# Performance work log

Hardware: AMD Instinct MI355X
Metric: run time of the kernel (lower is better)

The kernel has to match this reference:

```python
import jax, jax.numpy as jnp
import numpy as np

A_DIM = 18
HID = 512
LSTM_IN = HID + A_DIM + 1  # 531


def setup_inputs() -> dict:
    key = jax.random.key(0)
    ks = jax.random.split(key, 26)
    T, B = 80, 64
    inp = {}
    inp["o"] = jax.random.randint(ks[0], (T, B, 1, 84, 84), 0, 255, dtype=jnp.int32)
    inp["a"] = jax.random.randint(ks[1], (T, B), 0, A_DIM, dtype=jnp.int32)
    inp["r"] = jax.random.normal(ks[2], (T, B), dtype=jnp.float32)
    inp["done"] = jax.random.randint(ks[3], (T, B), 0, 2, dtype=jnp.int32)
    inp["h0"] = jnp.zeros((B, HID), dtype=jnp.float32)
    inp["c0"] = jnp.zeros((B, HID), dtype=jnp.float32)

    def gw(k, shape, s=0.05):
        return (jax.random.normal(k, shape, dtype=jnp.float32) * s)

    # CNN trunk params (torch Conv2d OIHW layout)
    inp["conv1_w"] = gw(ks[4], (32, 1, 8, 8))
    inp["conv1_b"] = jnp.zeros((32,), jnp.float32)
    inp["conv2_w"] = gw(ks[5], (64, 32, 4, 4))
    inp["conv2_b"] = jnp.zeros((64,), jnp.float32)
    inp["conv3_w"] = gw(ks[6], (64, 64, 3, 3))
    inp["conv3_b"] = jnp.zeros((64,), jnp.float32)
    inp["fc_w"] = gw(ks[7], (HID, 64 * 7 * 7))
    inp["fc_b"] = jnp.zeros((HID,), jnp.float32)
    # LSTM params (torch gate order: i, f, g, o)
    inp["W_ih"] = gw(ks[8], (4 * HID, LSTM_IN))
    inp["W_hh"] = gw(ks[9], (4 * HID, HID))
    inp["b_ih"] = jnp.zeros((4 * HID,), jnp.float32)
    inp["b_hh"] = jnp.zeros((4 * HID,), jnp.float32)
    # Dueling heads
    inp["adv_w1"] = gw(ks[10], (HID, HID))
    inp["adv_b1"] = jnp.zeros((HID,), jnp.float32)
    inp["adv_w2"] = gw(ks[11], (A_DIM, HID))
    inp["adv_b2"] = jnp.zeros((A_DIM,), jnp.float32)
    inp["val_w1"] = gw(ks[12], (HID, HID))
    inp["val_b1"] = jnp.zeros((HID,), jnp.float32)
    inp["val_w2"] = gw(ks[13], (1, HID))
    inp["val_b2"] = jnp.zeros((1,), jnp.float32)
    return inp


def _conv(x, w, b, stride):
    y = jax.lax.conv_general_dilated(
        x, w, (stride, stride), 'VALID',
        dimension_numbers=('NCHW', 'OIHW', 'NCHW'))
    return y + b[None, :, None, None]


def reference(o, a, r, done, h0, c0,
              conv1_w, conv1_b, conv2_w, conv2_b, conv3_w, conv3_b,
              fc_w, fc_b, W_ih, W_hh, b_ih, b_hh,
              adv_w1, adv_b1, adv_w2, adv_b2,
              val_w1, val_b1, val_w2, val_b2):
    T, B = o.shape[0], o.shape[1]
    x = o.reshape(T * B, 1, 84, 84).astype(jnp.float32) / 255.0
    x = jax.nn.relu(_conv(x, conv1_w, conv1_b, 4))   # [TB,32,20,20]
    x = jax.nn.relu(_conv(x, conv2_w, conv2_b, 2))   # [TB,64,9,9]
    x = jax.nn.relu(_conv(x, conv3_w, conv3_b, 1))   # [TB,64,7,7]
    x = x.reshape(T * B, 64 * 7 * 7)
    hidden = jax.nn.relu(x @ fc_w.T + fc_b).reshape(T, B, HID)

    a_one_hot = jax.nn.one_hot(a, A_DIM, dtype=jnp.float32)      # [T,B,A]
    lstm_in = jnp.concatenate([hidden, r[..., None], a_one_hot], axis=-1)  # [T,B,531]
    keep = (1.0 - done.astype(jnp.float32))[..., None]           # [T,B,1]
    bias = b_ih + b_hh

    def step(carry, inp_t):
        h, c = carry
        x_t, m = inp_t
        h = h * m
        c = c * m
        g = x_t @ W_ih.T + h @ W_hh.T + bias   # [B, 4H]
        i, f, gg, oo = jnp.split(g, 4, axis=-1)
        c = jax.nn.sigmoid(f) * c + jax.nn.sigmoid(i) * jnp.tanh(gg)
        h = jax.nn.sigmoid(oo) * jnp.tanh(c)
        return (h, c), h

    (hT, cT), hs = jax.lax.scan(step, (h0, c0), (lstm_in, keep))
    z = hs.reshape(T * B, HID)

    adv = jax.nn.relu(z @ adv_w1.T + adv_b1) @ adv_w2.T + adv_b2  # [TB,A]
    val = jax.nn.relu(z @ val_w1.T + val_b1) @ val_w2.T + val_b2  # [TB,1]
    q = val + (adv - adv.mean(axis=1, keepdims=True))
    return q.reshape(T, B, A_DIM), hT, cT
```

## Files before the change

### kernel.cpp

```cpp
#include <hip/hip_runtime.h>
#include <hip/hip_bf16.h>
#include <stdint.h>

typedef __bf16 bf16;
typedef __bf16 bfrag __attribute__((ext_vector_type(8)));
typedef short s16x8 __attribute__((ext_vector_type(8)));
typedef float f32x4 __attribute__((ext_vector_type(4)));
typedef float f32x16 __attribute__((ext_vector_type(16)));
typedef uint32_t u32x4 __attribute__((ext_vector_type(4)));

#define DEV __device__ __forceinline__

DEV bfrag ldg16(const bf16* p){ return *(const bfrag*)p; }

struct U64x2 { uint64_t a, b; };
DEV bfrag ld2x8(const bf16* p){
  U64x2 t; t.a = *(const uint64_t*)p; t.b = *(const uint64_t*)(p+4);
  return __builtin_bit_cast(bfrag, t);
}

DEV f32x4  mfma16(bfrag a, bfrag b, f32x4  c){ return __builtin_amdgcn_mfma_f32_16x16x32_bf16(a,b,c,0,0,0); }
DEV f32x16 mfma32(bfrag a, bfrag b, f32x16 c){ return __builtin_amdgcn_mfma_f32_32x32x16_bf16(a,b,c,0,0,0); }

DEV f32x16 zero16(){
  f32x16 v;
  for(int i=0;i<16;++i) v[i]=0.f;
  return v;
}
DEV f32x4 zero4(){
  f32x4 v;
  for(int i=0;i<4;++i) v[i]=0.f;
  return v;
}

DEV float sigm(float x){ return 1.0f/(1.0f+__expf(-x)); }
DEV float ftanh(float x){ float e = __expf(2.f*x); return 1.f - 2.f/(e+1.f); }

DEV u32x4 ldcg4(const uint32_t* p){
  u32x4 r;
  asm volatile("global_load_dwordx4 %0, %1, off sc0 sc1" : "=v"(r) : "v"(p));
  return r;
}

DEV uint32_t pk2f(float a, float b){
  bf16 x = (bf16)a, y = (bf16)b;
  return (uint32_t)__builtin_bit_cast(uint16_t,x) | ((uint32_t)__builtin_bit_cast(uint16_t,y)<<16);
}

DEV void gl_lds16(const bf16* g, void* l){
  __builtin_amdgcn_global_load_lds(
      (const __attribute__((address_space(1))) uint32_t*)g,
      (__attribute__((address_space(3))) uint32_t*)l, 16, 0, 0);
}

__global__ __launch_bounds__(256) void k_prep(
    const float* __restrict__ c1w, const float* __restrict__ c2w,
    const float* __restrict__ c3w, const float* __restrict__ fcw,
    const float* __restrict__ Wih, const float* __restrict__ WhhF,
    const float* __restrict__ bih, const float* __restrict__ bhh,
    const float* __restrict__ aw1, const float* __restrict__ aw2,
    const float* __restrict__ vw1, const float* __restrict__ vw2,
    const float* __restrict__ h0, const float* __restrict__ ab1,
    const float* __restrict__ vb1,
    bf16* w1b, bf16* w2r, bf16* w3r, bf16* fcwr, bf16* Wx, bf16* Whh,
    float* biasL, float* Wr, float* Wa, bf16* headw1, float* headb1,
    bf16* w2cat, uint32_t* hcurT)
{
  long i = (long)blockIdx.x*256 + threadIdx.x;
  if (i < 2048){ int co=(int)(i>>6), k=(int)(i&63);
    w1b[i] = (bf16)(c1w[co*64+k]*(1.f/255.f)); return; } i -= 2048;
  if (i < 32768){ int o=(int)(i>>9), k=(int)(i&511);
    int ky=k>>7, kx=(k>>5)&3, ci=k&31;
    w2r[i] = (bf16)c2w[((o*32+ci)*4+ky)*4+kx]; return; } i -= 32768;
  if (i < 36864){ int o=(int)(i/576), k=(int)(i%576);
    int ky=k/192, rem=k-ky*192, kx=rem>>6, ci=rem&63;
    w3r[i] = (bf16)c3w[((o*64+ci)*3+ky)*3+kx]; return; } i -= 36864;
  if (i < 1605632){
    int o=(int)(i/3136), rem=(int)(i%3136);
    int ci=rem/49, yx=rem-ci*49, y=yx/7, x=yx-y*7;
    fcwr[o*3200 + y*448 + x*64 + ci] = (bf16)fcw[i]; return; } i -= 1605632;
  if (i < 32768){ int o=(int)(i>>6), k=(int)(i&63);
    fcwr[o*3200 + 3136 + k] = (bf16)0.f; return; } i -= 32768;
  if (i < 1048576){ int n=(int)(i>>9), k=(int)(i&511);
    Wx[i] = (bf16)Wih[n*531+k]; return; } i -= 1048576;
  if (i < 1048576){ int n=(int)(i>>9), k=(int)(i&511);
    Whh[i] = (bf16)WhhF[n*512+k]; return; } i -= 1048576;
  if (i < 2048){ biasL[i] = bih[i]+bhh[i]; return; } i -= 2048;
  if (i < 2048){ Wr[i] = Wih[i*531+512]; return; } i -= 2048;
  if (i < 36864){ int j=(int)(i>>11), n=(int)(i&2047);
    Wa[i] = Wih[n*531+513+j]; return; } i -= 36864;
  if (i < 524288){ headw1[i] = (bf16)(i<262144 ? aw1[i] : vw1[i-262144]); return; } i -= 524288;
  if (i < 1024){ headb1[i] = (i<512) ? ab1[i] : vb1[i-512]; return; } i -= 1024;
  if (i < 32768){ int n=(int)(i>>10), k=(int)(i&1023);
    float v = 0.f;
    if (n<18 && k<512) v = aw2[n*512+k];
    else if (n==18 && k>=512) v = vw2[k-512];
    w2cat[i] = (bf16)v; return; } i -= 32768;
  if (i < 32768){
    if (i < 16384){
      int row = (int)(i>>8), wd = (int)(i&255);
      uint32_t pk = pk2f(h0[row*512 + wd*2], h0[row*512 + wd*2 + 1]);
      hcurT[i] = pk & ~0x00010001u;
    } else {
      hcurT[i] = 0x00010000u;
    }
    return;
  }
}

__global__ __launch_bounds__(256,2) void k_conv12(
    const int* __restrict__ o, const bf16* __restrict__ w1b,
    const float* __restrict__ c1b, const bf16* __restrict__ w2r,
    const float* __restrict__ c2b, bf16* __restrict__ act2)
{
  __shared__ bf16 lact[2][16000];
  const int tid = threadIdx.x;
  const int w = tid>>6, l = tid&63;
  const int img = w>>1, h = w&1;
  const long gimg = (long)blockIdx.x*2 + img;
  const int* ip = o + gimg*7056;
  char* lw = (char*)&lact[img][0];
  {
    bfrag bw[4];
    #pragma unroll
    for (int ks=0;ks<4;++ks) bw[ks] = ldg16(w1b + (l&31)*64 + ks*16 + 8*(l>>5));
    const float bias = c1b[l&31];
    for (int mt=h; mt<13; mt+=2){
      f32x16 acc = zero16();
      int m0 = mt*32 + (l&31);
      int p  = m0>399 ? 399 : m0;
      int oy = p/20, ox = p - oy*20;
      #pragma unroll
      for (int ks=0;ks<4;++ks){
        int ky = 2*ks + (l>>5);
        const int* q = ip + (oy*4+ky)*84 + ox*4;
        int4 i0 = *(const int4*)q;
        int4 i1 = *(const int4*)(q+4);
        bfrag a;
        a[0]=(bf16)(float)i0.x; a[1]=(bf16)(float)i0.y;
        a[2]=(bf16)(float)i0.z; a[3]=(bf16)(float)i0.w;
        a[4]=(bf16)(float)i1.x; a[5]=(bf16)(float)i1.y;
        a[6]=(bf16)(float)i1.z; a[7]=(bf16)(float)i1.w;
        acc = mfma32(a, bw[ks], acc);
      }
      #pragma unroll
      for (int r2=0;r2<16;++r2){
        int row = (r2&3) + 8*(r2>>2) + 4*(l>>5);
        int m = mt*32 + row;
        if (m < 400){
          float v = acc[r2] + bias; v = v>0.f ? v : 0.f;
          *(bf16*)(lw + m*80 + (l&31)*2) = (bf16)v;
        }
      }
    }
  }
  __syncthreads();
  {
    f32x16 acc2[3];
    #pragma unroll
    for (int a2=0;a2<3;++a2) acc2[a2]=zero16();
    int pb[3];
    #pragma unroll
    for (int mt=0;mt<3;++mt){
      int m = mt*32 + (l&31); int p = m>80 ? 80 : m;
      int oy = p/9, ox = p - oy*9;
      pb[mt] = (oy*2)*20 + ox*2;
    }
    #pragma unroll 4
    for (int ks=0; ks<32; ++ks){
      int k  = ks*16 + 8*(l>>5);
      int ky = k>>7, kx = (k>>5)&3, ci = k&31;
      bfrag b0 = ldg16(w2r + (32*h + (l&31))*512 + k);
      #pragma unroll
      for (int mt=0; mt<3; ++mt){
        int p2 = pb[mt] + ky*20 + kx;
        bfrag a = *(const bfrag*)(lw + p2*80 + ci*2);
        acc2[mt] = mfma32(a, b0, acc2[mt]);
      }
    }
    const float bias2 = c2b[32*h + (l&31)];
    #pragma unroll
    for (int mt=0; mt<3; ++mt){
      #pragma unroll
      for (int r2=0;r2<16;++r2){
        int row = (r2&3) + 8*(r2>>2) + 4*(l>>5);
        int m = mt*32 + row;
        if (m < 81){
          float v = acc2[mt][r2] + bias2; v = v>0.f ? v : 0.f;
          act2[gimg*5184 + m*64 + 32*h + (l&31)] = (bf16)v;
        }
      }
    }
  }
}

__global__ __launch_bounds__(256,2) void k_conv3(
    const bf16* __restrict__ act2, const bf16* __restrict__ w3r,
    const float* __restrict__ c3b, bf16* __restrict__ act3)
{
  const int tid=threadIdx.x, w=tid>>6, l=tid&63;
  const long img = (long)blockIdx.x*4 + w;
  const bf16* A = act2 + img*5184;
  f32x16 acc[2][2];
  #pragma unroll
  for(int a2=0;a2<2;++a2){ acc[a2][0]=zero16(); acc[a2][1]=zero16(); }
  #pragma unroll 4
  for (int ks=0; ks<36; ++ks){
    int k  = ks*16 + 8*(l>>5);
    int ky = k/192, rem = k - ky*192, kx = rem>>6, ci = rem&63;
    bfrag b0 = ldg16(w3r + (l&31)*576 + k);
    bfrag b1 = ldg16(w3r + (32+(l&31))*576 + k);
    #pragma unroll
    for (int mt=0; mt<2; ++mt){
      int m = mt*32 + (l&31); int p = m>48 ? 48 : m;
      int oy = p/7, ox = p - oy*7;
      bfrag a = ldg16(A + ((oy+ky)*9 + (ox+kx))*64 + ci);
      acc[mt][0] = mfma32(a, b0, acc[mt][0]);
      acc[mt][1] = mfma32(a, b1, acc[mt][1]);
    }
  }
  const float bias0 = c3b[l&31], bias1 = c3b[32+(l&31)];
  #pragma unroll
  for (int mt=0; mt<2; ++mt){
    #pragma unroll
    for (int r2=0;r2<16;++r2){
      int row = (r2&3) + 8*(r2>>2) + 4*(l>>5);
      int m = mt*32 + row;
      if (m < 50){
        float v0 = 0.f, v1 = 0.f;
        if (m < 49){
          v0 = acc[mt][0][r2] + bias0; v0 = v0>0.f ? v0 : 0.f;
          v1 = acc[mt][1][r2] + bias1; v1 = v1>0.f ? v1 : 0.f;
        }
        act3[img*3200 + m*64 + (l&31)]      = (bf16)v0;
        act3[img*3200 + m*64 + 32 + (l&31)] = (bf16)v1;
      }
    }
  }
}

template<bool RELU, bool OUTBF16>
__global__ __launch_bounds__(256,4) void k_gemm(
    const bf16* __restrict__ A, long lda,
    const bf16* __restrict__ W, long ldb,
    const float* __restrict__ bias,
    float* __restrict__ outF, bf16* __restrict__ outB, long ldo, int K,
    const float* __restrict__ fixR, const int* __restrict__ fixA,
    const float* __restrict__ fixWr, const float* __restrict__ fixWa)
{
  __shared__ bf16 sA[8192];
  char* sb = (char*)sA;
  const int tid=threadIdx.x, w=tid>>6, l=tid&63;
  const int m0 = blockIdx.x*64, n0 = blockIdx.y*128;
  f32x16 acc[2]; acc[0]=zero16(); acc[1]=zero16();
  const int mt = w&1;
  const int rowa = mt*32 + (l&31);
  for (int kc=0; kc<K; kc+=128){
    __syncthreads();
    #pragma unroll
    for (int j=0;j<4;++j){
      int idx = j*64 + l;
      int row = w*16 + (idx>>4);
      int seg = idx&15;
      const bf16* gp = A + (long)(m0+row)*lda + kc + (((seg*16) ^ ((row&15)<<4))>>1);
      gl_lds16(gp, sb + w*4096 + j*1024);
    }
    asm volatile("s_waitcnt vmcnt(0)" ::: "memory");
    __syncthreads();
    #pragma unroll
    for (int ks=0; ks<8; ++ks){
      bfrag a = *(const bfrag*)(sb + rowa*256 + ((ks*32 + (l>>5)*16) ^ ((rowa&15)<<4)));
      #pragma unroll
      for (int j=0;j<2;++j){
        int nt = (w>>1)*2 + j;
        bfrag b = ldg16(W + (long)(n0 + nt*32 + (l&31))*ldb + kc + ks*16 + 8*(l>>5));
        acc[j] = mfma32(a, b, acc[j]);
      }
    }
  }
  #pragma unroll
  for (int j=0;j<2;++j){
    int nt = (w>>1)*2 + j;
    int gc = n0 + nt*32 + (l&31);
    float bv = bias ? bias[gc] : 0.f;
    float wrv = fixR ? fixWr[gc] : 0.f;
    #pragma unroll
    for (int r2=0;r2<16;++r2){
      int row = (r2&3) + 8*(r2>>2) + 4*(l>>5);
      long gr = m0 + mt*32 + row;
      float v = acc[j][r2] + bv;
      if (fixR) v += fixR[gr]*wrv + fixWa[(long)fixA[gr]*2048 + gc];
      if (RELU) v = v>0.f ? v : 0.f;
      if (OUTBF16) outB[gr*ldo + gc] = (bf16)v;
      else         outF[gr*ldo + gc] = v;
    }
  }
}

__global__ __launch_bounds__(256,1) void k_lstm(
    const bf16* __restrict__ G, const int* __restrict__ done,
    const float* __restrict__ c0, const bf16* __restrict__ Whh,
    uint32_t* __restrict__ hcurT, bf16* __restrict__ hseq,
    float* __restrict__ outH, float* __restrict__ outC)
{
  __shared__ bf16 sh2[8192];
  __shared__ float sg[4][16][33];
  __shared__ float sc[16][33];
  __shared__ char  sdone[80][16];
  const int tid=threadIdx.x, w=tid>>6, l=tid&63;
  const int blk=blockIdx.x;
  const int grp=(blk&7)>>1, jj=((blk&1)<<3)|(blk>>3);
  const int bb = grp*16, uu = jj*32;

  for (int p=tid; p<512; p+=256){ int m=p>>5, u=p&31; sc[m][u] = c0[(bb+m)*512 + uu + u]; }
  for (int p=tid; p<1280; p+=256){ int t=p>>4, m=p&15; sdone[t][m] = (char)done[t*64 + bb + m]; }

  bfrag wb0[16], wb1[16];
  {
    const long row0 = (long)w*512 + uu + (l&15);
    #pragma unroll
    for (int ks=0; ks<16; ++ks){
      int k = ks*32 + 8*(l>>4);
      wb0[ks] = ldg16(Whh + row0*512 + k);
      wb1[ks] = ldg16(Whh + (row0+16)*512 + k);
      asm volatile("" : "+v"(wb0[ks]), "+v"(wb1[ks]));
    }
  }

  char* shb = (char*)sh2;
  const int loff = l*16;
  const int srow  = tid>>4;
  const int sci   = tid&15;

  __syncthreads();

  for (int t=0; t<80; ++t){
    float gv0[4], gv1[4];
    {
      const bf16* Gt = G + ((long)t*64 + bb)*2048 + w*512 + uu;
      #pragma unroll
      for (int r2=0;r2<4;++r2){
        int m2 = (l>>4)*4 + r2;
        gv0[r2] = (float)Gt[(long)m2*2048 + (l&15)];
        gv1[r2] = (float)Gt[(long)m2*2048 + 16 + (l&15)];
      }
    }
    __builtin_amdgcn_sched_barrier(0);
    {
      const uint32_t* hb = hcurT + (size_t)(t&1)*16384 + (size_t)(bb+srow)*256 + sci*16;
      u32x4 hv[4];
      const uint32_t expPat = ((uint32_t)(t&1)) | (((uint32_t)((t>>1)&1))<<16);
      for (;;){
        #pragma unroll
        for (int j2=0;j2<4;++j2) hv[j2] = ldcg4(hb + j2*4);
        asm volatile("s_waitcnt vmcnt(0)" ::: "memory");
        bool ok = true;
        #pragma unroll
        for (int j2=0;j2<4;++j2){
          ok &= ((hv[j2][0]&0x00010001u)==expPat) & ((hv[j2][1]&0x00010001u)==expPat)
              & ((hv[j2][2]&0x00010001u)==expPat) & ((hv[j2][3]&0x00010001u)==expPat);
        }
        if (__all(ok)) break;
        __builtin_amdgcn_s_sleep(1);
      }
      if (sdone[t][srow]){
        #pragma unroll
        for (int j2=0;j2<4;++j2){ u32x4 z = {0,0,0,0}; hv[j2] = z; }
      } else {
        #pragma unroll
        for (int j2=0;j2<4;++j2){
          hv[j2][0] &= ~0x00010001u; hv[j2][1] &= ~0x00010001u;
          hv[j2][2] &= ~0x00010001u; hv[j2][3] &= ~0x00010001u;
        }
      }
      #pragma unroll
      for (int j=0;j<4;++j){
        *(u32x4*)(shb + sci*1024 + ((((srow + 16*j)*16)) ^ ((sci&7)<<4))) = hv[j];
      }
    }
    __syncthreads();
    f32x4 a0e = zero4(), a0o = zero4(), a1e = zero4(), a1o = zero4();
    #pragma unroll
    for (int ks=0; ks<16; ++ks){
      bfrag a = *(const bfrag*)(shb + ks*1024 + (loff ^ ((ks&7)<<4)));
      if (ks & 1){ a0o = mfma16(a, wb0[ks], a0o); a1o = mfma16(a, wb1[ks], a1o); }
      else       { a0e = mfma16(a, wb0[ks], a0e); a1e = mfma16(a, wb1[ks], a1e); }
    }
    #pragma unroll
    for (int r2=0;r2<4;++r2){
      int m = (l>>4)*4 + r2;
      sg[w][m][(l&15)]    = a0e[r2] + a0o[r2] + gv0[r2];
      sg[w][m][16+(l&15)] = a1e[r2] + a1o[r2] + gv1[r2];
    }
    __syncthreads();
    {
      int p0 = tid*2; int m = p0>>5, u = p0&31;
      int dn = sdone[t][m];
      float c_0 = dn ? 0.f : sc[m][u];
      float c_1 = dn ? 0.f : sc[m][u+1];
      float i0=sg[0][m][u],   f0=sg[1][m][u],   g0=sg[2][m][u],   o0=sg[3][m][u];
      float i1=sg[0][m][u+1], f1=sg[1][m][u+1], g1=sg[2][m][u+1], o1=sg[3][m][u+1];
      float cn0 = sigm(f0)*c_0 + sigm(i0)*ftanh(g0);
      float cn1 = sigm(f1)*c_1 + sigm(i1)*ftanh(g1);
      float h_0 = sigm(o0)*ftanh(cn0);
      float h_1 = sigm(o1)*ftanh(cn1);
      sc[m][u] = cn0; sc[m][u+1] = cn1;
      uint32_t pk = pk2f(h_0, h_1);
      int p1 = (t+1)&3;
      uint32_t pat = ((uint32_t)(p1&1)) | (((uint32_t)(p1>>1))<<16);
      uint32_t pkT = (pk & ~0x00010001u) | pat;
      __hip_atomic_store(
          hcurT + (size_t)((t+1)&1)*16384 + (size_t)(bb+m)*256 + ((uu+u)>>1),
          pkT, __ATOMIC_RELAXED, __HIP_MEMORY_SCOPE_AGENT);
      *(uint32_t*)(hseq + ((long)t*64 + bb + m)*512 + uu + u) = pk;
      if (t == 79){
        outH[(bb+m)*512 + uu + u]   = h_0;  outH[(bb+m)*512 + uu + u+1] = h_1;
        outC[(bb+m)*512 + uu + u]   = cn0;  outC[(bb+m)*512 + uu + u+1] = cn1;
      }
    }
  }
}

__global__ __launch_bounds__(256) void k_qhead(
    const bf16* __restrict__ zav, const bf16* __restrict__ w2cat,
    const float* __restrict__ ab2, const float* __restrict__ vb2,
    float* __restrict__ q)
{
  __shared__ float sq[4][16][33];
  const int tid=threadIdx.x, w=tid>>6, l=tid&63;
  const int s0 = blockIdx.x*64 + w*16;
  f32x4 acc0 = zero4(), acc1 = zero4();
  const int row = l&15;
  #pragma unroll 4
  for (int ks=0; ks<32; ++ks){
    int k = ks*32 + 8*(l>>4);
    bfrag a  = ldg16(zav + (long)(s0+row)*1024 + k);
    bfrag b0 = ldg16(w2cat + (l&15)*1024 + k);
    bfrag b1 = ldg16(w2cat + (16+(l&15))*1024 + k);
    acc0 = mfma16(a, b0, acc0);
    acc1 = mfma16(a, b1, acc1);
  }
  #pragma unroll
  for (int r2=0;r2<4;++r2){
    int m = (l>>4)*4 + r2;
    sq[w][m][l&15]      = acc0[r2];
    sq[w][m][16+(l&15)] = acc1[r2];
  }
  __syncthreads();
  if (l < 16){
    int s = s0 + l;
    float av[18]; float sum = 0.f;
    #pragma unroll
    for (int j=0;j<18;++j){ av[j] = sq[w][l][j] + ab2[j]; sum += av[j]; }
    float val = sq[w][l][18] + vb2[0];
    float mean = sum * (1.f/18.f);
    #pragma unroll
    for (int j=0;j<18;++j) q[(long)s*18 + j] = val + av[j] - mean;
  }
}

extern "C" void kernel_launch(void* const* d_in, const int* in_sizes, int n_in,
                              void* d_out, int out_size, void* d_ws, size_t ws_size,
                              hipStream_t stream)
{
  (void)in_sizes; (void)n_in; (void)out_size;
  const int*   o_in = (const int*)  d_in[0];
  const int*   a_in = (const int*)  d_in[1];
  const float* r_in = (const float*)d_in[2];
  const int*   done = (const int*)  d_in[3];
  const float* h0   = (const float*)d_in[4];
  const float* c0   = (const float*)d_in[5];
  const float* c1w  = (const float*)d_in[6],  *c1b=(const float*)d_in[7];
  const float* c2w  = (const float*)d_in[8],  *c2b=(const float*)d_in[9];
  const float* c3w  = (const float*)d_in[10], *c3b=(const float*)d_in[11];
  const float* fcw  = (const float*)d_in[12], *fcb=(const float*)d_in[13];
  const float* Wih  = (const float*)d_in[14], *WhhF=(const float*)d_in[15];
  const float* bih  = (const float*)d_in[16], *bhh=(const float*)d_in[17];
  const float* aw1  = (const float*)d_in[18], *ab1=(const float*)d_in[19];
  const float* aw2  = (const float*)d_in[20], *ab2=(const float*)d_in[21];
  const float* vw1  = (const float*)d_in[22], *vb1=(const float*)d_in[23];
  const float* vw2  = (const float*)d_in[24], *vb2=(const float*)d_in[25];

  char* ws = (char*)d_ws;
  size_t off = 0;
  auto alloc = [&](size_t b){ size_t p = off; off = (off + b + 255) & ~(size_t)255; return p; };
  bf16*  act2   = (bf16*) (ws + alloc(53084160));
  bf16*  act3   = (bf16*) (ws + alloc(32768000));
  bf16*  hidden = (bf16*) (ws + alloc(5242880));
  uint32_t* hcurT = (uint32_t*)(ws + alloc(131072));
  bf16*  w1b    = (bf16*) (ws + alloc(4096));
  bf16*  w2r    = (bf16*) (ws + alloc(65536));
  bf16*  w3r    = (bf16*) (ws + alloc(73728));
  bf16*  fcwr   = (bf16*) (ws + alloc(3276800));
  bf16*  Wx     = (bf16*) (ws + alloc(2097152));
  bf16*  Whh    = (bf16*) (ws + alloc(2097152));
  float* biasL  = (float*)(ws + alloc(8192));
  float* Wr     = (float*)(ws + alloc(8192));
  float* Wa     = (float*)(ws + alloc(147456));
  bf16*  headw1 = (bf16*) (ws + alloc(1048576));
  float* headb1 = (float*)(ws + alloc(4096));
  bf16*  w2cat  = (bf16*) (ws + alloc(65536));
  if (off > ws_size) return;

  bf16*  G    = act2;
  bf16*  hseq = hidden;
  bf16*  zav  = act3;

  float* qout = (float*)d_out;
  float* outH = qout + 92160;
  float* outC = qout + 124928;

  k_prep<<<17340, 256, 0, stream>>>(c1w, c2w, c3w, fcw, Wih, WhhF, bih, bhh,
      aw1, aw2, vw1, vw2, h0, ab1, vb1, w1b, w2r, w3r, fcwr, Wx, Whh,
      biasL, Wr, Wa, headw1, headb1, w2cat, hcurT);

  k_conv12<<<2560, 256, 0, stream>>>(o_in, w1b, c1b, w2r, c2b, act2);
  k_conv3<<<1280, 256, 0, stream>>>(act2, w3r, c3b, act3);
  k_gemm<true,true><<<dim3(80,4), 256, 0, stream>>>(
      act3, 3200, fcwr, 3200, fcb, nullptr, hidden, 512, 3200,
      nullptr, nullptr, nullptr, nullptr);
  k_gemm<false,true><<<dim3(80,16), 256, 0, stream>>>(
      hidden, 512, Wx, 512, biasL, nullptr, G, 2048, 512,
      r_in, a_in, Wr, Wa);

  k_lstm<<<64, 256, 0, stream>>>(G, done, c0, Whh, hcurT, hseq, outH, outC);

  k_gemm<true,true><<<dim3(80,8), 256, 0, stream>>>(
      hseq, 512, headw1, 512, headb1, nullptr, zav, 1024, 512,
      nullptr, nullptr, nullptr, nullptr);
  k_qhead<<<80, 256, 0, stream>>>(zav, w2cat, ab2, vb2, qout);
}
```

Before: 603.6 us.

## Remap LSTM gate columns per wave to compute cell update in registers

Each wave's MFMA output columns are remapped so that a lane pair (xor 8) holds the i/f and g/o gates for the same hidden unit. The cell state now lives in registers and the gate exchange uses shuffles instead of a shared-memory staging buffer, which removes one __syncthreads per timestep. The h shared buffer is double-buffered by timestep parity so the next step's staging does not race with reads from the current step. In exchange, half the lanes sit idle during the packed stores, and the row ordering of the W_hh and G loads changes.

Result: slower. 754.4 us (median of 2 runs) (+25.0%).

```diff
diff --git a/kernel.cpp b/kernel.cpp
--- a/kernel.cpp
+++ b/kernel.cpp
@@ -303,31 +303,37 @@
     uint32_t* __restrict__ hcurT, bf16* __restrict__ hseq,
     float* __restrict__ outH, float* __restrict__ outC)
 {
-  __shared__ bf16 sh2[8192];
-  __shared__ float sg[4][16][33];
-  __shared__ float sc[16][33];
+  __shared__ bf16 sh2[2][8192];
   __shared__ char  sdone[80][16];
   const int tid=threadIdx.x, w=tid>>6, l=tid&63;
   const int blk=blockIdx.x;
   const int grp=(blk&7)>>1, jj=((blk&1)<<3)|(blk>>3);
   const int bb = grp*16, uu = jj*32;
-
-  for (int p=tid; p<512; p+=256){ int m=p>>5, u=p&31; sc[m][u] = c0[(bb+m)*512 + uu + u]; }
+  const int w8 = w*8;
+  const int x  = l&15;
+
   for (int p=tid; p<1280; p+=256){ int t=p>>4, m=p&15; sdone[t][m] = (char)done[t*64 + bb + m]; }
+
+  float creg[4];
+  #pragma unroll
+  for (int r2=0;r2<4;++r2){
+    int m = (l>>4)*4 + r2;
+    creg[r2] = c0[(bb+m)*512 + uu + w8 + (x&7)];
+  }
 
   bfrag wb0[16], wb1[16];
   {
-    const long row0 = (long)w*512 + uu + (l&15);
+    const long row0 = (long)((x>>3))*512 + uu + w8 + (x&7);
+    const long row1 = row0 + 1024;
     #pragma unroll
     for (int ks=0; ks<16; ++ks){
       int k = ks*32 + 8*(l>>4);
       wb0[ks] = ldg16(Whh + row0*512 + k);
-      wb1[ks] = ldg16(Whh + (row0+16)*512 + k);
+      wb1[ks] = ldg16(Whh + row1*512 + k);
       asm volatile("" : "+v"(wb0[ks]), "+v"(wb1[ks]));
     }
   }
 
-  char* shb = (char*)sh2;
   const int loff = l*16;
   const int srow  = tid>>4;
   const int sci   = tid&15;
@@ -337,15 +343,17 @@
   for (int t=0; t<80; ++t){
     float gv0[4], gv1[4];
     {
-      const bf16* Gt = G + ((long)t*64 + bb)*2048 + w*512 + uu;
+      const bf16* Gt = G + ((long)t*64 + bb)*2048;
+      const int col0 = ((x>>3)<<9) + uu + w8 + (x&7);
       #pragma unroll
       for (int r2=0;r2<4;++r2){
         int m2 = (l>>4)*4 + r2;
-        gv0[r2] = (float)Gt[(long)m2*2048 + (l&15)];
-        gv1[r2] = (float)Gt[(long)m2*2048 + 16 + (l&15)];
+        gv0[r2] = (float)Gt[(long)m2*2048 + col0];
+        gv1[r2] = (float)Gt[(long)m2*2048 + col0 + 1024];
       }
     }
     __builtin_amdgcn_sched_barrier(0);
+    char* shb = (char*)&sh2[t&1][0];
     {
       const uint32_t* hb = hcurT + (size_t)(t&1)*16384 + (size_t)(bb+srow)*256 + sci*16;
       u32x4 hv[4];
@@ -386,36 +394,41 @@
       if (ks & 1){ a0o = mfma16(a, wb0[ks], a0o); a1o = mfma16(a, wb1[ks], a1o); }
       else       { a0e = mfma16(a, wb0[ks], a0e); a1e = mfma16(a, wb1[ks], a1e); }
     }
-    #pragma unroll
-    for (int r2=0;r2<4;++r2){
-      int m = (l>>4)*4 + r2;
-      sg[w][m][(l&15)]    = a0e[r2] + a0o[r2] + gv0[r2];
-      sg[w][m][16+(l&15)] = a1e[r2] + a1o[r2] + gv1[r2];
-    }
-    __syncthreads();
     {
-      int p0 = tid*2; int m = p0>>5, u = p0&31;
-      int dn = sdone[t][m];
-      float c_0 = dn ? 0.f : sc[m][u];
-      float c_1 = dn ? 0.f : sc[m][u+1];
-      float i0=sg[0][m][u],   f0=sg[1][m][u],   g0=sg[2][m][u],   o0=sg[3][m][u];
-      float i1=sg[0][m][u+1], f1=sg[1][m][u+1], g1=sg[2][m][u+1], o1=sg[3][m][u+1];
-      float cn0 = sigm(f0)*c_0 + sigm(i0)*ftanh(g0);
-      float cn1 = sigm(f1)*c_1 + sigm(i1)*ftanh(g1);
-      float h_0 = sigm(o0)*ftanh(cn0);
-      float h_1 = sigm(o1)*ftanh(cn1);
-      sc[m][u] = cn0; sc[m][u+1] = cn1;
-      uint32_t pk = pk2f(h_0, h_1);
-      int p1 = (t+1)&3;
-      uint32_t pat = ((uint32_t)(p1&1)) | (((uint32_t)(p1>>1))<<16);
-      uint32_t pkT = (pk & ~0x00010001u) | pat;
-      __hip_atomic_store(
-          hcurT + (size_t)((t+1)&1)*16384 + (size_t)(bb+m)*256 + ((uu+u)>>1),
-          pkT, __ATOMIC_RELAXED, __HIP_MEMORY_SCOPE_AGENT);
-      *(uint32_t*)(hseq + ((long)t*64 + bb + m)*512 + uu + u) = pk;
-      if (t == 79){
-        outH[(bb+m)*512 + uu + u]   = h_0;  outH[(bb+m)*512 + uu + u+1] = h_1;
-        outC[(bb+m)*512 + uu + u]   = cn0;  outC[(bb+m)*512 + uu + u+1] = cn1;
+      const int p1 = (t+1)&3;
+      const uint32_t pat = ((uint32_t)(p1&1)) | (((uint32_t)(p1>>1))<<16);
+      #pragma unroll
+      for (int r2=0;r2<4;++r2){
+        int m = (l>>4)*4 + r2;
+        float v0 = a0e[r2] + a0o[r2] + gv0[r2];
+        float v1 = a1e[r2] + a1o[r2] + gv1[r2];
+        float p0 = __shfl_xor(v0, 8);
+        float p1f = __shfl_xor(v1, 8);
+        float gi = (x&8)? p0  : v0;
+        float gf = (x&8)? v0  : p0;
+        float gg = (x&8)? p1f : v1;
+        float go = (x&8)? v1  : p1f;
+        int dn = sdone[t][m];
+        float cprev = dn ? 0.f : creg[r2];
+        float cn = sigm(gf)*cprev + sigm(gi)*ftanh(gg);
+        float hh = sigm(go)*ftanh(cn);
+        creg[r2] = cn;
+        float hq = __shfl_xor(hh, 1);
+        if (!(x&8)){
+          int u = uu + w8 + (x&7);
+          if (!(x&1)){
+            uint32_t pk  = pk2f(hh, hq);
+            uint32_t pkT = (pk & ~0x00010001u) | pat;
+            __hip_atomic_store(
+                hcurT + (size_t)((t+1)&1)*16384 + (size_t)(bb+m)*256 + (u>>1),
+                pkT, __ATOMIC_RELAXED, __HIP_MEMORY_SCOPE_AGENT);
+            *(uint32_t*)(hseq + ((long)t*64 + bb + m)*512 + u) = pk;
+          }
+          if (t == 79){
+            outH[(bb+m)*512 + u] = hh;
+            outC[(bb+m)*512 + u] = cn;
+          }
+        }
       }
     }
   }
```
